# Performance work log

Measured on AMD Instinct MI355X. Metric: run time of the kernel, lower is better.

## Reference

```python
import jax, jax.numpy as jnp
import numpy as np

B, G, T, D = 512, 10, 100, 50
H, EMB, NEMB, OUT = 30, 20, 10, 10


def _gru_last_hidden(x, W_ih, W_hh, b_ih, b_hh):
    """PyTorch-convention GRU over x:[N,T,D]; returns final hidden [N,H].
    Gate order in the 3H dim is (r, z, n), matching torch.nn.GRU."""
    N = x.shape[0]
    # precompute input projections for all timesteps: [N,T,3H] -> [T,N,3H]
    xw = jnp.einsum('ntd,gd->ntg', x, W_ih) + b_ih
    xw = jnp.swapaxes(xw, 0, 1)
    h0 = jnp.zeros((N, H), dtype=x.dtype)

    def step(h, xw_t):
        gh = h @ W_hh.T + b_hh                      # [N,3H]
        r = jax.nn.sigmoid(xw_t[:, :H] + gh[:, :H])
        z = jax.nn.sigmoid(xw_t[:, H:2 * H] + gh[:, H:2 * H])
        n = jnp.tanh(xw_t[:, 2 * H:] + r * gh[:, 2 * H:])
        h = (1.0 - z) * n + z * h
        return h, None

    hT, _ = jax.lax.scan(step, h0, xw)
    return hT


def setup_inputs() -> dict:
    key = jax.random.key(0)
    ks = jax.random.split(key, 12)
    s_g = 1.0 / np.sqrt(H)
    inp = {
        'input1': jax.random.normal(ks[0], (B, G, T, D), jnp.float32),
        'input2': jax.random.normal(ks[1], (B, G, T, D), jnp.float32),
        'W_ih': jax.random.normal(ks[2], (3 * H, D), jnp.float32) * s_g,
        'W_hh': jax.random.normal(ks[3], (3 * H, H), jnp.float32) * s_g,
        'b_ih': jax.random.normal(ks[4], (3 * H,), jnp.float32) * s_g,
        'b_hh': jax.random.normal(ks[5], (3 * H,), jnp.float32) * s_g,
        'W1': jax.random.normal(ks[6], (EMB, H * G), jnp.float32) / np.sqrt(H * G),
        'b1': jax.random.normal(ks[7], (EMB,), jnp.float32) * 0.01,
        'W2': jax.random.normal(ks[8], (NEMB, EMB), jnp.float32) / np.sqrt(EMB),
        'b2': jax.random.normal(ks[9], (NEMB,), jnp.float32) * 0.01,
        'W3': jax.random.normal(ks[10], (OUT, NEMB), jnp.float32) / np.sqrt(NEMB),
        'b3': jax.random.normal(ks[11], (OUT,), jnp.float32) * 0.01,
    }
    return inp


def reference(input1, input2, W_ih, W_hh, b_ih, b_hh, W1, b1, W2, b2, W3, b3):
    gelu = lambda v: jax.nn.gelu(v, approximate=False)  # torch GELU default = exact
    # Fuse all num_gru slices of both inputs into one big batched GRU call
    x = jnp.concatenate([input1, input2], axis=0).reshape(2 * B * G, T, D)
    hT = _gru_last_hidden(x, W_ih, W_hh, b_ih, b_hh)    # [2BG, H]
    h = hT.reshape(2, B, G * H)                          # cat over num_gru == reshape
    embeddings1, embeddings2 = h[0], h[1]               # random_dis, MLP input
    logit_emb = gelu(embeddings2 @ W1.T + b1) @ W2.T + b2
    logit = gelu(logit_emb) @ W3.T + b3
    return logit, embeddings1
```

## Files before the change

kernel.cpp:

```cpp
#include <hip/hip_runtime.h>
#include <hip/hip_bf16.h>
#include <math.h>

#define T_    100
#define D_    50
#define H_    30
#define HALF  5120
#define EMB_  20
#define NEMB_ 10
#define OUT_  10

typedef _Float16 h2    __attribute__((ext_vector_type(2)));
typedef _Float16 f16x8 __attribute__((ext_vector_type(8)));
typedef float    f32x4 __attribute__((ext_vector_type(4)));

union FR  { f16x8 v; h2 p[4]; float4 f4; };

__device__ __forceinline__ h2 pk(float a, float b) {
    return __builtin_bit_cast(h2, __builtin_amdgcn_cvt_pkrtz(a, b));
}
__device__ __forceinline__ int pki(float a, float b) {
    return __builtin_bit_cast(int, __builtin_amdgcn_cvt_pkrtz(a, b));
}

#if __has_builtin(__builtin_amdgcn_exp2f)
#define EXP2(x) __builtin_amdgcn_exp2f(x)
#else
#define EXP2(x) exp2f(x)
#endif

struct XR { float2 a0, a1, a2, a3, b0, b1, b2, b3; };

__global__ __launch_bounds__(64, 1) void gru_kernel(
    const float* __restrict__ input1, const float* __restrict__ input2,
    const float* __restrict__ W_ih,  const float* __restrict__ W_hh,
    const float* __restrict__ b_ih,  const float* __restrict__ b_hh,
    float* __restrict__ emb1_out,
    float* __restrict__ h2_out)
{
    const int lane = threadIdx.x & 63;
    const int s    = lane & 15;
    const int q    = lane >> 4;
    const int n    = blockIdx.x * 16 + s;

    __shared__ __align__(16) _Float16 Wst [96 * 64];
    __shared__ __align__(16) _Float16 Whst[96 * 32];

    const float SC_RZ = -1.4426950408889634f;
    const float SC_N  =  2.8853900817779268f;

    for (int i = lane; i < 1536; i += 64) ((unsigned long long*)Wst)[i]  = 0ull;
    for (int i = lane; i < 768;  i += 64) ((unsigned long long*)Whst)[i] = 0ull;

    for (int i = 0; i < 71; ++i) {
        int idx = lane + i * 64;
        if (idx < 4500) {
            int rw = idx / 50, k = idx - rw * 50;
            int g  = rw / 30;
            int ge = rw + 2 * g;
            float sc = (g < 2) ? SC_RZ : SC_N;
            Wst[ge * 64 + k] = (_Float16)(W_ih[idx] * sc);
        }
    }
    for (int i = 0; i < 2; ++i) {
        int idx = lane + i * 64;
        if (idx < 90) {
            int g = idx / 30; int ge = idx + 2 * g;
            float sc = (g < 2) ? SC_RZ : SC_N;
            Wst[ge * 64 + 50] = (_Float16)(b_ih[idx] * sc);
        }
    }
    for (int i = 0; i < 43; ++i) {
        int idx = lane + i * 64;
        if (idx < 2700) {
            int rw = idx / 30, k = idx - rw * 30;
            int g  = rw / 30;
            int ge = rw + 2 * g;
            float sc = (g < 2) ? SC_RZ : SC_N;
            Whst[ge * 32 + k] = (_Float16)(W_hh[idx] * sc);
        }
    }
    for (int i = 0; i < 2; ++i) {
        int idx = lane + i * 64;
        if (idx < 90) {
            int g = idx / 30; int ge = idx + 2 * g;
            float sc = (g < 2) ? SC_RZ : SC_N;
            Whst[ge * 32 + 30] = (_Float16)(b_hh[idx] * sc);
        }
    }
    __syncthreads();

    FR wih[6][2], whh[6];
    #pragma unroll
    for (int nt = 0; nt < 6; ++nt) {
        wih[nt][0].f4 = *(const float4*)&Wst [(nt * 16 + s) * 64 + q * 8];
        wih[nt][1].f4 = *(const float4*)&Wst [(nt * 16 + s) * 64 + 32 + q * 8];
        whh[nt].f4    = *(const float4*)&Whst[(nt * 16 + s) * 32 + q * 8];
    }

    const float* xp = (n < HALF) ? input1 + (size_t)n * (T_ * D_)
                                 : input2 + (size_t)(n - HALF) * (T_ * D_);

    auto load_x = [&](int t, XR& X) {
        const float* r  = xp + t * D_;
        const float* pa = r + q * 8;
        const float* pb = (q < 2) ? (r + 32 + q * 8) : r;
        const float* p0 = (q == 2) ? (r + 48) : pb;
        X.a0 = *(const float2*)(pa + 0);
        X.a1 = *(const float2*)(pa + 2);
        X.a2 = *(const float2*)(pa + 4);
        X.a3 = *(const float2*)(pa + 6);
        X.b0 = *(const float2*)(p0);
        X.b1 = *(const float2*)(pb + 2);
        X.b2 = *(const float2*)(pb + 4);
        X.b3 = *(const float2*)(pb + 6);
    };
    auto build = [&](const XR& X, FR& x0, FR& x1) {
        x0.p[0] = pk(X.a0.x, X.a0.y); x0.p[1] = pk(X.a1.x, X.a1.y);
        x0.p[2] = pk(X.a2.x, X.a2.y); x0.p[3] = pk(X.a3.x, X.a3.y);
        if (q < 2) {
            x1.p[0] = pk(X.b0.x, X.b0.y); x1.p[1] = pk(X.b1.x, X.b1.y);
            x1.p[2] = pk(X.b2.x, X.b2.y); x1.p[3] = pk(X.b3.x, X.b3.y);
        } else if (q == 2) {
            x1.p[0] = pk(X.b0.x, X.b0.y); x1.p[1] = pk(1.f, 0.f);
            x1.p[2] = pk(0.f, 0.f);       x1.p[3] = pk(0.f, 0.f);
        } else {
            x1.p[0] = pk(0.f, 0.f); x1.p[1] = pk(0.f, 0.f);
            x1.p[2] = pk(0.f, 0.f); x1.p[3] = pk(0.f, 0.f);
        }
    };

    float hold[8] = {0.f, 0.f, 0.f, 0.f, 0.f, 0.f, 0.f, 0.f};
    int w0 = 0, w1 = 0, w2 = 0, w3 = 0;
    const int la = ((2 * q) & 3) * 16 + s;
    const int lb = ((2 * q + 1) & 3) * 16 + s;
    const int ONE = pki(1.f, 0.f);

    auto step = [&](const FR& x0, const FR& x1) {
        const int A0 = __shfl(w0, la), A1 = __shfl(w1, la);
        const int A2 = __shfl(w2, la), A3 = __shfl(w3, la);
        const int B0 = __shfl(w0, lb), B1 = __shfl(w1, lb);
        const int B2 = __shfl(w2, lb), B3 = __shfl(w3, lb);
        FR bh;
        bh.p[0] = __builtin_bit_cast(h2, q < 2 ? A0 : A2);
        bh.p[1] = __builtin_bit_cast(h2, q < 2 ? A1 : A3);
        bh.p[2] = __builtin_bit_cast(h2, q < 2 ? B0 : B2);
        bh.p[3] = __builtin_bit_cast(h2, q == 3 ? ONE : (q < 2 ? B1 : B3));

        f32x4 arz[4], anh[2], anx[2];
        #pragma unroll
        for (int nt = 0; nt < 4; ++nt) {
            f32x4 acc = {0.f, 0.f, 0.f, 0.f};
            acc = __builtin_amdgcn_mfma_f32_16x16x32_f16(wih[nt][0].v, x0.v, acc, 0, 0, 0);
            acc = __builtin_amdgcn_mfma_f32_16x16x32_f16(wih[nt][1].v, x1.v, acc, 0, 0, 0);
            acc = __builtin_amdgcn_mfma_f32_16x16x32_f16(whh[nt].v,    bh.v, acc, 0, 0, 0);
            arz[nt] = acc;
        }
        #pragma unroll
        for (int u = 0; u < 2; ++u) {
            f32x4 ax = {0.f, 0.f, 0.f, 0.f}, ah = {0.f, 0.f, 0.f, 0.f};
            ax = __builtin_amdgcn_mfma_f32_16x16x32_f16(wih[4 + u][0].v, x0.v, ax, 0, 0, 0);
            ax = __builtin_amdgcn_mfma_f32_16x16x32_f16(wih[4 + u][1].v, x1.v, ax, 0, 0, 0);
            ah = __builtin_amdgcn_mfma_f32_16x16x32_f16(whh[4 + u].v,    bh.v, ah, 0, 0, 0);
            anh[u] = ah; anx[u] = ax;
        }
        #pragma unroll
        for (int u = 0; u < 2; ++u) {
            #pragma unroll
            for (int r = 0; r < 4; ++r) {
                const float rg = __builtin_amdgcn_rcpf(1.f + EXP2(arz[u][r]));
                const float zg = __builtin_amdgcn_rcpf(1.f + EXP2(arz[2 + u][r]));
                const float aa = fmaf(rg, anh[u][r], anx[u][r]);
                const float th = fmaf(-2.f, __builtin_amdgcn_rcpf(1.f + EXP2(aa)), 1.f);
                hold[u * 4 + r] = fmaf(zg, hold[u * 4 + r] - th, th);
            }
        }
        w0 = pki(hold[0], hold[1]); w1 = pki(hold[2], hold[3]);
        w2 = pki(hold[4], hold[5]); w3 = pki(hold[6], hold[7]);
    };

    XR X0, X1, X2, X3, X4, X5, X6, X7;
    load_x(0, X0); load_x(1, X1); load_x(2, X2); load_x(3, X3);
    load_x(4, X4); load_x(5, X5); load_x(6, X6); load_x(7, X7);
    #pragma unroll 1
    for (int k = 0; k < 12; ++k) {
        const int t = 8 * k;
        FR x0, x1;
        build(X0, x0, x1); load_x(t +  8 < 100 ? t +  8 : 99, X0); step(x0, x1);
        build(X1, x0, x1); load_x(t +  9 < 100 ? t +  9 : 99, X1); step(x0, x1);
        build(X2, x0, x1); load_x(t + 10 < 100 ? t + 10 : 99, X2); step(x0, x1);
        build(X3, x0, x1); load_x(t + 11 < 100 ? t + 11 : 99, X3); step(x0, x1);
        build(X4, x0, x1); load_x(t + 12 < 100 ? t + 12 : 99, X4); step(x0, x1);
        build(X5, x0, x1); load_x(t + 13 < 100 ? t + 13 : 99, X5); step(x0, x1);
        build(X6, x0, x1); load_x(t + 14 < 100 ? t + 14 : 99, X6); step(x0, x1);
        build(X7, x0, x1); load_x(t + 15 < 100 ? t + 15 : 99, X7); step(x0, x1);
    }
    {
        FR x0, x1;
        build(X0, x0, x1); step(x0, x1);
        build(X1, x0, x1); step(x0, x1);
        build(X2, x0, x1); step(x0, x1);
        build(X3, x0, x1); step(x0, x1);
    }

    float* outp = (n < HALF) ? emb1_out + (size_t)n * H_
                             : h2_out + (size_t)(n - HALF) * H_;
    #pragma unroll
    for (int u = 0; u < 2; ++u)
        #pragma unroll
        for (int r = 0; r < 4; ++r) {
            const int j = 16 * u + 4 * q + r;
            if (j < H_) outp[j] = hold[u * 4 + r];
        }
}

__global__ __launch_bounds__(64) void mlp_kernel(
    const float* __restrict__ h2i,
    const float* __restrict__ W1, const float* __restrict__ b1,
    const float* __restrict__ W2, const float* __restrict__ b2,
    const float* __restrict__ W3, const float* __restrict__ b3,
    float* __restrict__ logit)
{
    const int b    = blockIdx.x;
    const int lane = threadIdx.x;
    __shared__ float e2[300];
    const float* row = h2i + (size_t)b * 300;
    #pragma unroll
    for (int i = lane; i < 75; i += 64)
        *(float4*)&e2[i * 4] = *(const float4*)(row + i * 4);
    __syncthreads();

    const float kInvSqrt2 = 0.70710678118654752f;
    float y1 = 0.f;
    if (lane < EMB_) {
        float acc = b1[lane];
        const float* wp = W1 + lane * 300;
        #pragma unroll
        for (int qq = 0; qq < 75; ++qq) {
            float4 wv = *(const float4*)(wp + qq * 4);
            acc += wv.x * e2[qq*4 + 0] + wv.y * e2[qq*4 + 1]
                 + wv.z * e2[qq*4 + 2] + wv.w * e2[qq*4 + 3];
        }
        y1 = 0.5f * acc * (1.f + erff(acc * kInvSqrt2));
    }
    float acc2 = (lane < NEMB_) ? b2[lane] : 0.f;
    #pragma unroll
    for (int e = 0; e < EMB_; ++e) {
        const float v = __shfl(y1, e);
        if (lane < NEMB_) acc2 += v * W2[lane * EMB_ + e];
    }
    const float y2 = 0.5f * acc2 * (1.f + erff(acc2 * kInvSqrt2));
    float acc3 = (lane < OUT_) ? b3[lane] : 0.f;
    #pragma unroll
    for (int e = 0; e < NEMB_; ++e) {
        const float v = __shfl(y2, e);
        if (lane < OUT_) acc3 += v * W3[lane * NEMB_ + e];
    }
    if (lane < OUT_) logit[(size_t)b * OUT_ + lane] = acc3;
}

extern "C" void kernel_launch(void* const* d_in, const int* in_sizes, int n_in,
                              void* d_out, int out_size, void* d_ws, size_t ws_size,
                              hipStream_t stream) {
    const float* input1 = (const float*)d_in[0];
    const float* input2 = (const float*)d_in[1];
    const float* W_ih   = (const float*)d_in[2];
    const float* W_hh   = (const float*)d_in[3];
    const float* b_ih   = (const float*)d_in[4];
    const float* b_hh   = (const float*)d_in[5];
    const float* W1     = (const float*)d_in[6];
    const float* b1     = (const float*)d_in[7];
    const float* W2     = (const float*)d_in[8];
    const float* b2     = (const float*)d_in[9];
    const float* W3     = (const float*)d_in[10];
    const float* b3     = (const float*)d_in[11];

    float* out = (float*)d_out;
    float* h2s = (float*)d_ws;

    hipLaunchKernelGGL(gru_kernel, dim3(640), dim3(64), 0, stream,
                       input1, input2, W_ih, W_hh, b_ih, b_hh,
                       out + 5120, h2s);
    hipLaunchKernelGGL(mlp_kernel, dim3(512), dim3(64), 0, stream,
                       h2s, W1, b1, W2, b2, W3, b3, out);
}
```

Before: 110.6 us.

## Use inline-asm dwordx4 loads with explicit vmcnt waits in GRU input prefetch

Replaces the eight float2 loads per timestep with four 16-byte global loads issued through inline assembly. A manual s_waitcnt vmcnt(12) before each use holds a four-deep ring of in-flight timestep buffers, replacing the compiler-managed eight-deep register prefetch. This cuts load instruction count and register pressure, and lets waits cover only the oldest buffer instead of relying on the compiler's conservative waitcnt placement. The EXP2 macro is also switched from the hardware exp2 builtin to exp2f, which may add instructions. Loads at odd timesteps are not 16-byte aligned. Correctness depends on the compiler not touching asm-output registers before the hand-placed waits.

```diff
diff --git a/kernel.cpp b/kernel.cpp
--- a/kernel.cpp
+++ b/kernel.cpp
@@ -23,13 +23,9 @@
     return __builtin_bit_cast(int, __builtin_amdgcn_cvt_pkrtz(a, b));
 }
 
-#if __has_builtin(__builtin_amdgcn_exp2f)
-#define EXP2(x) __builtin_amdgcn_exp2f(x)
-#else
 #define EXP2(x) exp2f(x)
-#endif
-
-struct XR { float2 a0, a1, a2, a3, b0, b1, b2, b3; };
+
+struct B4 { float4 A0, A1, B0, B1; };
 
 __global__ __launch_bounds__(64, 1) void gru_kernel(
     const float* __restrict__ input1, const float* __restrict__ input2,
@@ -101,28 +97,30 @@
     const float* xp = (n < HALF) ? input1 + (size_t)n * (T_ * D_)
                                  : input2 + (size_t)(n - HALF) * (T_ * D_);
 
-    auto load_x = [&](int t, XR& X) {
-        const float* r  = xp + t * D_;
-        const float* pa = r + q * 8;
-        const float* pb = (q < 2) ? (r + 32 + q * 8) : r;
-        const float* p0 = (q == 2) ? (r + 48) : pb;
-        X.a0 = *(const float2*)(pa + 0);
-        X.a1 = *(const float2*)(pa + 2);
-        X.a2 = *(const float2*)(pa + 4);
-        X.a3 = *(const float2*)(pa + 6);
-        X.b0 = *(const float2*)(p0);
-        X.b1 = *(const float2*)(pb + 2);
-        X.b2 = *(const float2*)(pb + 4);
-        X.b3 = *(const float2*)(pb + 6);
-    };
-    auto build = [&](const XR& X, FR& x0, FR& x1) {
-        x0.p[0] = pk(X.a0.x, X.a0.y); x0.p[1] = pk(X.a1.x, X.a1.y);
-        x0.p[2] = pk(X.a2.x, X.a2.y); x0.p[3] = pk(X.a3.x, X.a3.y);
+    const int aoff = q * 8;
+    const int boff = (q < 2) ? (32 + q * 8) : 42;
+
+    auto issue_load = [&](int t, B4& b) {
+        const float* pa = xp + t * D_ + aoff;
+        const float* pb = xp + t * D_ + boff;
+        asm volatile("global_load_dwordx4 %0, %1, off"           : "=v"(b.A0) : "v"(pa));
+        asm volatile("global_load_dwordx4 %0, %1, off offset:16" : "=v"(b.A1) : "v"(pa));
+        asm volatile("global_load_dwordx4 %0, %1, off"           : "=v"(b.B0) : "v"(pb));
+        asm volatile("global_load_dwordx4 %0, %1, off offset:16" : "=v"(b.B1) : "v"(pb));
+    };
+    auto wait_buf = [&]() {
+        asm volatile("s_waitcnt vmcnt(12)" ::: "memory");
+        __builtin_amdgcn_sched_barrier(0);
+    };
+
+    auto build = [&](const B4& X, FR& x0, FR& x1) {
+        x0.p[0] = pk(X.A0.x, X.A0.y); x0.p[1] = pk(X.A0.z, X.A0.w);
+        x0.p[2] = pk(X.A1.x, X.A1.y); x0.p[3] = pk(X.A1.z, X.A1.w);
         if (q < 2) {
-            x1.p[0] = pk(X.b0.x, X.b0.y); x1.p[1] = pk(X.b1.x, X.b1.y);
-            x1.p[2] = pk(X.b2.x, X.b2.y); x1.p[3] = pk(X.b3.x, X.b3.y);
+            x1.p[0] = pk(X.B0.x, X.B0.y); x1.p[1] = pk(X.B0.z, X.B0.w);
+            x1.p[2] = pk(X.B1.x, X.B1.y); x1.p[3] = pk(X.B1.z, X.B1.w);
         } else if (q == 2) {
-            x1.p[0] = pk(X.b0.x, X.b0.y); x1.p[1] = pk(1.f, 0.f);
+            x1.p[0] = pk(X.B1.z, X.B1.w); x1.p[1] = pk(1.f, 0.f);
             x1.p[2] = pk(0.f, 0.f);       x1.p[3] = pk(0.f, 0.f);
         } else {
             x1.p[0] = pk(0.f, 0.f); x1.p[1] = pk(0.f, 0.f);
@@ -179,29 +177,24 @@
         w2 = pki(hold[4], hold[5]); w3 = pki(hold[6], hold[7]);
     };
 
-    XR X0, X1, X2, X3, X4, X5, X6, X7;
-    load_x(0, X0); load_x(1, X1); load_x(2, X2); load_x(3, X3);
-    load_x(4, X4); load_x(5, X5); load_x(6, X6); load_x(7, X7);
+    B4 Bf0, Bf1, Bf2, Bf3;
+    issue_load(0, Bf0); issue_load(1, Bf1);
+    issue_load(2, Bf2); issue_load(3, Bf3);
     #pragma unroll 1
-    for (int k = 0; k < 12; ++k) {
-        const int t = 8 * k;
+    for (int k = 0; k < 25; ++k) {
+        const int t = 4 * k;
         FR x0, x1;
-        build(X0, x0, x1); load_x(t +  8 < 100 ? t +  8 : 99, X0); step(x0, x1);
-        build(X1, x0, x1); load_x(t +  9 < 100 ? t +  9 : 99, X1); step(x0, x1);
-        build(X2, x0, x1); load_x(t + 10 < 100 ? t + 10 : 99, X2); step(x0, x1);
-        build(X3, x0, x1); load_x(t + 11 < 100 ? t + 11 : 99, X3); step(x0, x1);
-        build(X4, x0, x1); load_x(t + 12 < 100 ? t + 12 : 99, X4); step(x0, x1);
-        build(X5, x0, x1); load_x(t + 13 < 100 ? t + 13 : 99, X5); step(x0, x1);
-        build(X6, x0, x1); load_x(t + 14 < 100 ? t + 14 : 99, X6); step(x0, x1);
-        build(X7, x0, x1); load_x(t + 15 < 100 ? t + 15 : 99, X7); step(x0, x1);
-    }
-    {
-        FR x0, x1;
-        build(X0, x0, x1); step(x0, x1);
-        build(X1, x0, x1); step(x0, x1);
-        build(X2, x0, x1); step(x0, x1);
-        build(X3, x0, x1); step(x0, x1);
-    }
+        int tn;
+        wait_buf(); build(Bf0, x0, x1);
+        tn = t + 4; tn = tn > 99 ? 99 : tn; issue_load(tn, Bf0); step(x0, x1);
+        wait_buf(); build(Bf1, x0, x1);
+        tn = t + 5; tn = tn > 99 ? 99 : tn; issue_load(tn, Bf1); step(x0, x1);
+        wait_buf(); build(Bf2, x0, x1);
+        tn = t + 6; tn = tn > 99 ? 99 : tn; issue_load(tn, Bf2); step(x0, x1);
+        wait_buf(); build(Bf3, x0, x1);
+        tn = t + 7; tn = tn > 99 ? 99 : tn; issue_load(tn, Bf3); step(x0, x1);
+    }
+    asm volatile("s_waitcnt vmcnt(0)" ::: "memory");
 
     float* outp = (n < HALF) ? emb1_out + (size_t)n * H_
                              : h2_out + (size_t)(n - HALF) * H_;
```

Result: slower. 142.0 us (+28.4%).

## Interleave two independent GRU sequences per wavefront to hide recurrence latency

Applied to the files above, without the earlier changes.

Each wavefront now processes two 16-sequence groups (A and B) and interleaves their recurrent steps, so the MFMA and transcendental latency of one chain can overlap the other. The grid is halved to 320 blocks and the prefetch depth drops from 8 timesteps to 2 per chain to save registers. EXP2 also switches from the amdgcn builtin to exp2f. Risks include more register pressure, less memory-latency hiding from the shallower prefetch, and fewer wavefronts to fill the 256 CUs.

```diff
diff --git a/kernel.cpp b/kernel.cpp
--- a/kernel.cpp
+++ b/kernel.cpp
@@ -23,11 +23,7 @@
     return __builtin_bit_cast(int, __builtin_amdgcn_cvt_pkrtz(a, b));
 }
 
-#if __has_builtin(__builtin_amdgcn_exp2f)
-#define EXP2(x) __builtin_amdgcn_exp2f(x)
-#else
 #define EXP2(x) exp2f(x)
-#endif
 
 struct XR { float2 a0, a1, a2, a3, b0, b1, b2, b3; };
 
@@ -41,7 +37,8 @@
     const int lane = threadIdx.x & 63;
     const int s    = lane & 15;
     const int q    = lane >> 4;
-    const int n    = blockIdx.x * 16 + s;
+    const int nA   = blockIdx.x * 32 + s;
+    const int nB   = nA + 16;
 
     __shared__ __align__(16) _Float16 Wst [96 * 64];
     __shared__ __align__(16) _Float16 Whst[96 * 32];
@@ -98,10 +95,12 @@
         whh[nt].f4    = *(const float4*)&Whst[(nt * 16 + s) * 32 + q * 8];
     }
 
-    const float* xp = (n < HALF) ? input1 + (size_t)n * (T_ * D_)
-                                 : input2 + (size_t)(n - HALF) * (T_ * D_);
-
-    auto load_x = [&](int t, XR& X) {
+    const float* xpA = (nA < HALF) ? input1 + (size_t)nA * (T_ * D_)
+                                   : input2 + (size_t)(nA - HALF) * (T_ * D_);
+    const float* xpB = (nB < HALF) ? input1 + (size_t)nB * (T_ * D_)
+                                   : input2 + (size_t)(nB - HALF) * (T_ * D_);
+
+    auto load_x = [&](const float* xp, int t, XR& X) {
         const float* r  = xp + t * D_;
         const float* pa = r + q * 8;
         const float* pb = (q < 2) ? (r + 32 + q * 8) : r;
@@ -130,13 +129,15 @@
         }
     };
 
-    float hold[8] = {0.f, 0.f, 0.f, 0.f, 0.f, 0.f, 0.f, 0.f};
-    int w0 = 0, w1 = 0, w2 = 0, w3 = 0;
+    float holdA[8] = {0.f, 0.f, 0.f, 0.f, 0.f, 0.f, 0.f, 0.f};
+    float holdB[8] = {0.f, 0.f, 0.f, 0.f, 0.f, 0.f, 0.f, 0.f};
+    int wA0 = 0, wA1 = 0, wA2 = 0, wA3 = 0;
+    int wB0 = 0, wB1 = 0, wB2 = 0, wB3 = 0;
     const int la = ((2 * q) & 3) * 16 + s;
     const int lb = ((2 * q + 1) & 3) * 16 + s;
     const int ONE = pki(1.f, 0.f);
 
-    auto step = [&](const FR& x0, const FR& x1) {
+    auto mkbh = [&](int w0, int w1, int w2, int w3) -> FR {
         const int A0 = __shfl(w0, la), A1 = __shfl(w1, la);
         const int A2 = __shfl(w2, la), A3 = __shfl(w3, la);
         const int B0 = __shfl(w0, lb), B1 = __shfl(w1, lb);
@@ -146,7 +147,11 @@
         bh.p[1] = __builtin_bit_cast(h2, q < 2 ? A1 : A3);
         bh.p[2] = __builtin_bit_cast(h2, q < 2 ? B0 : B2);
         bh.p[3] = __builtin_bit_cast(h2, q == 3 ? ONE : (q < 2 ? B1 : B3));
-
+        return bh;
+    };
+
+    auto core = [&](const FR& x0, const FR& x1, const FR& bh,
+                    float (&hold)[8], int& w0, int& w1, int& w2, int& w3) {
         f32x4 arz[4], anh[2], anx[2];
         #pragma unroll
         for (int nt = 0; nt < 4; ++nt) {
@@ -179,38 +184,43 @@
         w2 = pki(hold[4], hold[5]); w3 = pki(hold[6], hold[7]);
     };
 
-    XR X0, X1, X2, X3, X4, X5, X6, X7;
-    load_x(0, X0); load_x(1, X1); load_x(2, X2); load_x(3, X3);
-    load_x(4, X4); load_x(5, X5); load_x(6, X6); load_x(7, X7);
+    XR XA0, XA1, XB0, XB1;
+    load_x(xpA, 0, XA0); load_x(xpB, 0, XB0);
+    load_x(xpA, 1, XA1); load_x(xpB, 1, XB1);
     #pragma unroll 1
-    for (int k = 0; k < 12; ++k) {
-        const int t = 8 * k;
-        FR x0, x1;
-        build(X0, x0, x1); load_x(t +  8 < 100 ? t +  8 : 99, X0); step(x0, x1);
-        build(X1, x0, x1); load_x(t +  9 < 100 ? t +  9 : 99, X1); step(x0, x1);
-        build(X2, x0, x1); load_x(t + 10 < 100 ? t + 10 : 99, X2); step(x0, x1);
-        build(X3, x0, x1); load_x(t + 11 < 100 ? t + 11 : 99, X3); step(x0, x1);
-        build(X4, x0, x1); load_x(t + 12 < 100 ? t + 12 : 99, X4); step(x0, x1);
-        build(X5, x0, x1); load_x(t + 13 < 100 ? t + 13 : 99, X5); step(x0, x1);
-        build(X6, x0, x1); load_x(t + 14 < 100 ? t + 14 : 99, X6); step(x0, x1);
-        build(X7, x0, x1); load_x(t + 15 < 100 ? t + 15 : 99, X7); step(x0, x1);
-    }
-    {
-        FR x0, x1;
-        build(X0, x0, x1); step(x0, x1);
-        build(X1, x0, x1); step(x0, x1);
-        build(X2, x0, x1); step(x0, x1);
-        build(X3, x0, x1); step(x0, x1);
-    }
-
-    float* outp = (n < HALF) ? emb1_out + (size_t)n * H_
-                             : h2_out + (size_t)(n - HALF) * H_;
+    for (int k = 0; k < 50; ++k) {
+        const int t = 2 * k;
+        FR a0, a1, b0, b1;
+        build(XA0, a0, a1); build(XB0, b0, b1);
+        { int tn = t + 2; tn = tn > 99 ? 99 : tn;
+          load_x(xpA, tn, XA0); load_x(xpB, tn, XB0); }
+        {
+            FR bhA = mkbh(wA0, wA1, wA2, wA3);
+            FR bhB = mkbh(wB0, wB1, wB2, wB3);
+            core(a0, a1, bhA, holdA, wA0, wA1, wA2, wA3);
+            core(b0, b1, bhB, holdB, wB0, wB1, wB2, wB3);
+        }
+        build(XA1, a0, a1); build(XB1, b0, b1);
+        { int tn = t + 3; tn = tn > 99 ? 99 : tn;
+          load_x(xpA, tn, XA1); load_x(xpB, tn, XB1); }
+        {
+            FR bhA = mkbh(wA0, wA1, wA2, wA3);
+            FR bhB = mkbh(wB0, wB1, wB2, wB3);
+            core(a0, a1, bhA, holdA, wA0, wA1, wA2, wA3);
+            core(b0, b1, bhB, holdB, wB0, wB1, wB2, wB3);
+        }
+    }
+
+    float* outA = (nA < HALF) ? emb1_out + (size_t)nA * H_
+                              : h2_out + (size_t)(nA - HALF) * H_;
+    float* outB = (nB < HALF) ? emb1_out + (size_t)nB * H_
+                              : h2_out + (size_t)(nB - HALF) * H_;
     #pragma unroll
     for (int u = 0; u < 2; ++u)
         #pragma unroll
         for (int r = 0; r < 4; ++r) {
             const int j = 16 * u + 4 * q + r;
-            if (j < H_) outp[j] = hold[u * 4 + r];
+            if (j < H_) { outA[j] = holdA[u * 4 + r]; outB[j] = holdB[u * 4 + r]; }
         }
 }
 
@@ -278,7 +288,7 @@
     float* out = (float*)d_out;
     float* h2s = (float*)d_ws;
 
-    hipLaunchKernelGGL(gru_kernel, dim3(640), dim3(64), 0, stream,
+    hipLaunchKernelGGL(gru_kernel, dim3(320), dim3(64), 0, stream,
                        input1, input2, W_ih, W_hh, b_ih, b_hh,
                        out + 5120, h2s);
     hipLaunchKernelGGL(mlp_kernel, dim3(512), dim3(64), 0, stream,
```

Measured after the change: 199.9 us. +80.7%, slower.

## Permute gate rows so MFMA output lands in B-operand layout, removing shuffles

Applied to the files above, without the earlier changes.

Reorders the hidden-unit rows of the staged W_ih/W_hh weights with a permutation so each lane's MFMA accumulator outputs are already in the positions needed for the next step's hidden-state B operand. This removes the eight cross-lane shuffles and selects on the serial recurrence critical path each timestep. The output store index is remapped to match. It also drops the amdgcn exp2 builtin in favour of plain exp2f, which may compile to slower code.

```diff
diff --git a/kernel.cpp b/kernel.cpp
--- a/kernel.cpp
+++ b/kernel.cpp
@@ -23,13 +23,13 @@
     return __builtin_bit_cast(int, __builtin_amdgcn_cvt_pkrtz(a, b));
 }
 
-#if __has_builtin(__builtin_amdgcn_exp2f)
-#define EXP2(x) __builtin_amdgcn_exp2f(x)
-#else
 #define EXP2(x) exp2f(x)
-#endif
 
 struct XR { float2 a0, a1, a2, a3, b0, b1, b2, b3; };
+
+__device__ __forceinline__ int rho(int j) {
+    return (j & 3) + 4 * (j >> 3) + 16 * ((j >> 2) & 1);
+}
 
 __global__ __launch_bounds__(64, 1) void gru_kernel(
     const float* __restrict__ input1, const float* __restrict__ input2,
@@ -56,8 +56,8 @@
         int idx = lane + i * 64;
         if (idx < 4500) {
             int rw = idx / 50, k = idx - rw * 50;
-            int g  = rw / 30;
-            int ge = rw + 2 * g;
+            int g  = rw / 30,  j = rw - g * 30;
+            int ge = g * 32 + rho(j);
             float sc = (g < 2) ? SC_RZ : SC_N;
             Wst[ge * 64 + k] = (_Float16)(W_ih[idx] * sc);
         }
@@ -65,7 +65,8 @@
     for (int i = 0; i < 2; ++i) {
         int idx = lane + i * 64;
         if (idx < 90) {
-            int g = idx / 30; int ge = idx + 2 * g;
+            int g = idx / 30, j = idx - g * 30;
+            int ge = g * 32 + rho(j);
             float sc = (g < 2) ? SC_RZ : SC_N;
             Wst[ge * 64 + 50] = (_Float16)(b_ih[idx] * sc);
         }
@@ -74,8 +75,8 @@
         int idx = lane + i * 64;
         if (idx < 2700) {
             int rw = idx / 30, k = idx - rw * 30;
-            int g  = rw / 30;
-            int ge = rw + 2 * g;
+            int g  = rw / 30,  j = rw - g * 30;
+            int ge = g * 32 + rho(j);
             float sc = (g < 2) ? SC_RZ : SC_N;
             Whst[ge * 32 + k] = (_Float16)(W_hh[idx] * sc);
         }
@@ -83,7 +84,8 @@
     for (int i = 0; i < 2; ++i) {
         int idx = lane + i * 64;
         if (idx < 90) {
-            int g = idx / 30; int ge = idx + 2 * g;
+            int g = idx / 30, j = idx - g * 30;
+            int ge = g * 32 + rho(j);
             float sc = (g < 2) ? SC_RZ : SC_N;
             Whst[ge * 32 + 30] = (_Float16)(b_hh[idx] * sc);
         }
@@ -132,20 +134,14 @@
 
     float hold[8] = {0.f, 0.f, 0.f, 0.f, 0.f, 0.f, 0.f, 0.f};
     int w0 = 0, w1 = 0, w2 = 0, w3 = 0;
-    const int la = ((2 * q) & 3) * 16 + s;
-    const int lb = ((2 * q + 1) & 3) * 16 + s;
     const int ONE = pki(1.f, 0.f);
 
     auto step = [&](const FR& x0, const FR& x1) {
-        const int A0 = __shfl(w0, la), A1 = __shfl(w1, la);
-        const int A2 = __shfl(w2, la), A3 = __shfl(w3, la);
-        const int B0 = __shfl(w0, lb), B1 = __shfl(w1, lb);
-        const int B2 = __shfl(w2, lb), B3 = __shfl(w3, lb);
         FR bh;
-        bh.p[0] = __builtin_bit_cast(h2, q < 2 ? A0 : A2);
-        bh.p[1] = __builtin_bit_cast(h2, q < 2 ? A1 : A3);
-        bh.p[2] = __builtin_bit_cast(h2, q < 2 ? B0 : B2);
-        bh.p[3] = __builtin_bit_cast(h2, q == 3 ? ONE : (q < 2 ? B1 : B3));
+        bh.p[0] = __builtin_bit_cast(h2, w0);
+        bh.p[1] = __builtin_bit_cast(h2, w1);
+        bh.p[2] = __builtin_bit_cast(h2, w2);
+        bh.p[3] = __builtin_bit_cast(h2, q == 3 ? ONE : w3);
 
         f32x4 arz[4], anh[2], anx[2];
         #pragma unroll
@@ -209,7 +205,7 @@
     for (int u = 0; u < 2; ++u)
         #pragma unroll
         for (int r = 0; r < 4; ++r) {
-            const int j = 16 * u + 4 * q + r;
+            const int j = 8 * q + 4 * u + r;
             if (j < H_) outp[j] = hold[u * 4 + r];
         }
 }
```

New measurement: 125.0 us. 13.0% more time.
